# Kernel optimization log

Measured on AMD Instinct MI355X. Metric: run time of the kernel, lower is better.

## Reference

```python
import jax, jax.numpy as jnp
import numpy as np

BN_EPS = 1e-5


def setup_inputs() -> dict:
    key = jax.random.key(0)
    ks = jax.random.split(key, 12)
    N, E = 100000, 400000
    node_in, hidden, L = 32, 128, 4
    x = jax.random.normal(ks[0], (N, node_in), dtype=jnp.float32)
    edge_index = jax.random.randint(ks[1], (2, E), 0, N, dtype=jnp.int32)
    s = 1.0 / np.sqrt(node_in)
    emb_W = jax.random.uniform(ks[2], (node_in, hidden), minval=-s, maxval=s, dtype=jnp.float32)
    emb_b = jax.random.uniform(ks[3], (hidden,), minval=-s, maxval=s, dtype=jnp.float32)
    s1 = 1.0 / np.sqrt(hidden)
    s2 = 1.0 / np.sqrt(2 * hidden)
    W1 = jax.random.uniform(ks[4], (L, hidden, 2 * hidden), minval=-s1, maxval=s1, dtype=jnp.float32)
    b1 = jax.random.uniform(ks[5], (L, 2 * hidden), minval=-s1, maxval=s1, dtype=jnp.float32)
    W2 = jax.random.uniform(ks[6], (L, 2 * hidden, hidden), minval=-s2, maxval=s2, dtype=jnp.float32)
    b2 = jax.random.uniform(ks[7], (L, hidden), minval=-s2, maxval=s2, dtype=jnp.float32)
    gamma = jnp.ones((L, hidden), dtype=jnp.float32)
    beta = jnp.zeros((L, hidden), dtype=jnp.float32)
    return {"x": x, "edge_index": edge_index, "emb_W": emb_W, "emb_b": emb_b,
            "W1": W1, "b1": b1, "W2": W2, "b2": b2, "gamma": gamma, "beta": beta}


def reference(x, edge_index, emb_W, emb_b, W1, b1, W2, b2, gamma, beta):
    # Node embedding: [N, node_in] @ [node_in, H] -> [N, H]
    h = x @ emb_W + emb_b
    src, dst = edge_index[0], edge_index[1]
    N = h.shape[0]
    L = W1.shape[0]
    for l in range(L):
        # GINConv (eps=0): sum-aggregate neighbor features then add self
        agg = jax.ops.segment_sum(h[src], dst, num_segments=N)  # [N, H]
        z = h + agg
        # 2-layer MLP: H -> 2H -> H with ReLU
        z = jax.nn.relu(z @ W1[l] + b1[l]) @ W2[l] + b2[l]
        # BatchNorm1d over nodes (training-mode batch statistics)
        mean = jnp.mean(z, axis=0)
        var = jnp.var(z, axis=0)
        z = (z - mean) * jax.lax.rsqrt(var + BN_EPS) * gamma[l] + beta[l]
        # ReLU (dropout is identity in eval mode)
        h = jax.nn.relu(z)
    return h
```

## Files before the change

kernel.cpp:

```cpp
#include <hip/hip_runtime.h>

#define H 128
#define H2 256
#define NODE_IN 32
#define BN_EPS 1e-5f

typedef __bf16 bf16x8 __attribute__((ext_vector_type(8)));
typedef __bf16 bf16x4 __attribute__((ext_vector_type(4)));
typedef float f32x4 __attribute__((ext_vector_type(4)));

#define MFMA(a, b, c) __builtin_amdgcn_mfma_f32_16x16x32_bf16(a, b, c, 0, 0, 0)

__global__ __launch_bounds__(256) void convert_weights_kernel(
    const float* __restrict__ W1, const float* __restrict__ W2,
    const float* __restrict__ embW, char* __restrict__ Ws, int L)
{
    int idx = blockIdx.x * 256 + threadIdx.x;
    int per = H * H2;
    int total = L * per;
    if (idx < total) {
        int l = idx / per, r = idx % per;
        int k = r / H2, n = r % H2;
        int c = k >> 3, e = k & 7;
        size_t off = (size_t)l * 131072 + n * 256 + (((c ^ (n & 7)) << 4)) + e * 2;
        *(__bf16*)(Ws + off) = (__bf16)W1[idx];
    } else if (idx < 2 * total) {
        int j = idx - total;
        int l = j / per, r = j % per;
        int k = r / H, n = r % H;
        int c = k >> 3, e = k & 7;
        size_t off = (size_t)l * 131072 + 65536 + n * 512 + (((c ^ (n & 7)) << 4)) + e * 2;
        *(__bf16*)(Ws + off) = (__bf16)W2[j];
    } else if (idx < 2 * total + H * NODE_IN) {
        int j = idx - 2 * total;
        int k = j / H, c = j % H;
        size_t off = (size_t)L * 131072 + c * 64 + k * 2;
        *(__bf16*)(Ws + off) = (__bf16)embW[j];
    }
}

__global__ __launch_bounds__(512) void embed_kernel(
    const float* __restrict__ x, const char* __restrict__ Wse,
    const float* __restrict__ bias, __bf16* __restrict__ h, int N)
{
    int tid = threadIdx.x;
    int w = tid >> 6, lane = tid & 63;
    int l15 = lane & 15, kg = lane >> 4;

    bf16x8 aw[8];
#pragma unroll
    for (int nt = 0; nt < 8; ++nt)
        aw[nt] = *(const bf16x8*)(Wse + (nt * 16 + l15) * 64 + kg * 16);

    int r = (blockIdx.x * 8 + w) * 16 + l15;
    bool ok = (r < N);

    bf16x8 xb = {};
    if (ok) {
        float4 v0 = *(const float4*)&x[(size_t)r * NODE_IN + kg * 8];
        float4 v1 = *(const float4*)&x[(size_t)r * NODE_IN + kg * 8 + 4];
        xb[0] = (__bf16)v0.x; xb[1] = (__bf16)v0.y;
        xb[2] = (__bf16)v0.z; xb[3] = (__bf16)v0.w;
        xb[4] = (__bf16)v1.x; xb[5] = (__bf16)v1.y;
        xb[6] = (__bf16)v1.z; xb[7] = (__bf16)v1.w;
    }

    __bf16* hr = h + (size_t)r * H;
#pragma unroll
    for (int nt = 0; nt < 8; ++nt) {
        f32x4 acc = {0.f, 0.f, 0.f, 0.f};
        acc = MFMA(aw[nt], xb, acc);
        if (ok) {
            float4 bb = *(const float4*)&bias[nt * 16 + kg * 4];
            bf16x4 hv;
            hv[0] = (__bf16)(acc[0] + bb.x);
            hv[1] = (__bf16)(acc[1] + bb.y);
            hv[2] = (__bf16)(acc[2] + bb.z);
            hv[3] = (__bf16)(acc[3] + bb.w);
            *(bf16x4*)(hr + nt * 16 + kg * 4) = hv;
        }
    }
}

__global__ __launch_bounds__(256) void hist_kernel(
    const int* __restrict__ dst, int* __restrict__ deg, int E)
{
    int e = blockIdx.x * 256 + threadIdx.x;
    if (e < E) atomicAdd(&deg[dst[e]], 1);
}

__global__ __launch_bounds__(256) void scan_partial_kernel(
    const int* __restrict__ deg, int* __restrict__ bsum, int N)
{
    __shared__ int red[256];
    int b = blockIdx.x, t = threadIdx.x;
    int base = b * 2048 + t * 8;
    int s = 0;
#pragma unroll
    for (int i = 0; i < 8; ++i) { int idx = base + i; if (idx < N) s += deg[idx]; }
    red[t] = s;
    __syncthreads();
    for (int d = 128; d > 0; d >>= 1) {
        if (t < d) red[t] += red[t + d];
        __syncthreads();
    }
    if (t == 0) bsum[b] = red[0];
}

__global__ __launch_bounds__(256) void scan_bsum_kernel(
    int* __restrict__ bsum, int* __restrict__ total, int numB)
{
    __shared__ int ts[256];
    int t = threadIdx.x;
    int v = (t < numB) ? bsum[t] : 0;
    ts[t] = v;
    __syncthreads();
    for (int d = 1; d < 256; d <<= 1) {
        int u = (t >= d) ? ts[t - d] : 0;
        __syncthreads();
        ts[t] += u;
        __syncthreads();
    }
    if (t < numB) bsum[t] = ts[t] - v;
    if (t == 255) *total = ts[255];
}

__global__ __launch_bounds__(256) void scan_apply_kernel(
    const int* __restrict__ deg, const int* __restrict__ bsum,
    int* __restrict__ offp, int* __restrict__ cursor, int N)
{
    __shared__ int ts[256];
    int b = blockIdx.x, t = threadIdx.x;
    int base = b * 2048 + t * 8;
    int loc[8];
    int s = 0;
#pragma unroll
    for (int i = 0; i < 8; ++i) {
        int idx = base + i;
        loc[i] = (idx < N) ? deg[idx] : 0;
        s += loc[i];
    }
    ts[t] = s;
    __syncthreads();
    for (int d = 1; d < 256; d <<= 1) {
        int u = (t >= d) ? ts[t - d] : 0;
        __syncthreads();
        ts[t] += u;
        __syncthreads();
    }
    int run = bsum[b] + ts[t] - s;
#pragma unroll
    for (int i = 0; i < 8; ++i) {
        int idx = base + i;
        if (idx < N) { offp[idx] = run; cursor[idx] = run; }
        run += loc[i];
    }
}

__global__ __launch_bounds__(256) void fill_kernel(
    const int* __restrict__ src, const int* __restrict__ dst,
    int* __restrict__ cursor, int* __restrict__ srclist, int E)
{
    int e = blockIdx.x * 256 + threadIdx.x;
    if (e < E) {
        int pos = atomicAdd(&cursor[dst[e]], 1);
        srclist[pos] = src[e];
    }
}

__device__ __forceinline__ uint32_t pack_relu2(float x, float y) {
    __bf16 a = (__bf16)fmaxf(x, 0.f), b = (__bf16)fmaxf(y, 0.f);
    return (uint32_t)__builtin_bit_cast(uint16_t, a) |
           ((uint32_t)__builtin_bit_cast(uint16_t, b) << 16);
}

template <int BN>
__global__ __launch_bounds__(512, 4) void gin_layer_kernel(
    const __bf16* __restrict__ hin, __bf16* __restrict__ hout,
    const float* __restrict__ ss,
    const int* __restrict__ offp, const int* __restrict__ srclist,
    const char* __restrict__ Ws, const float* __restrict__ b1l,
    const float* __restrict__ b2l, float* __restrict__ spart, int N)
{
    __shared__ __align__(16) char zt[16384];
    __shared__ __align__(16) char hl[32768];
    __shared__ float sstat[256];

    int tid = threadIdx.x;
    int w = tid >> 6, lane = tid & 63;
    int l15 = lane & 15, kg = lane >> 4;
    const int xsw = (l15 & 7) << 4;
    int r0g = blockIdx.x * 64;

    if (tid < 256) sstat[tid] = 0.f;

    bf16x8 aW1[2][4];
#pragma unroll
    for (int nt = 0; nt < 2; ++nt)
#pragma unroll
        for (int kk = 0; kk < 4; ++kk)
            aW1[nt][kk] = *(const bf16x8*)(
                Ws + (w * 32 + nt * 16 + l15) * 256 + ((((kk * 4 + kg) << 4)) ^ xsw));
    float4 bb1[2];
#pragma unroll
    for (int nt = 0; nt < 2; ++nt)
        bb1[nt] = *(const float4*)&b1l[w * 32 + nt * 16 + kg * 4];

    {
        float sc[8], sh[8];
        if (BN) {
#pragma unroll
            for (int j = 0; j < 8; ++j) {
                sc[j] = ss[l15 * 8 + j];
                sh[j] = ss[H + l15 * 8 + j];
            }
        }
#pragma unroll
        for (int p = 0; p < 2; ++p) {
            int rl = w * 8 + p * 4 + kg;
            int r = r0g + rl;
            bf16x8 o = {};
            if (r < N) {
                float acc[8];
                bf16x8 sv = *(const bf16x8*)(hin + (size_t)r * H + l15 * 8);
#pragma unroll
                for (int j = 0; j < 8; ++j) {
                    float f = (float)sv[j];
                    acc[j] = BN ? fmaxf(f * sc[j] + sh[j], 0.f) : f;
                }
                int i0 = offp[r], i1 = offp[r + 1];
                int i = i0;
                for (; i + 3 < i1; i += 4) {
                    int s0 = srclist[i], s1 = srclist[i + 1];
                    int s2 = srclist[i + 2], s3 = srclist[i + 3];
                    bf16x8 u0 = *(const bf16x8*)(hin + (size_t)s0 * H + l15 * 8);
                    bf16x8 u1 = *(const bf16x8*)(hin + (size_t)s1 * H + l15 * 8);
                    bf16x8 u2 = *(const bf16x8*)(hin + (size_t)s2 * H + l15 * 8);
                    bf16x8 u3 = *(const bf16x8*)(hin + (size_t)s3 * H + l15 * 8);
#pragma unroll
                    for (int j = 0; j < 8; ++j) {
                        float f0 = (float)u0[j], f1 = (float)u1[j];
                        float f2 = (float)u2[j], f3 = (float)u3[j];
                        if (BN) {
                            f0 = fmaxf(f0 * sc[j] + sh[j], 0.f);
                            f1 = fmaxf(f1 * sc[j] + sh[j], 0.f);
                            f2 = fmaxf(f2 * sc[j] + sh[j], 0.f);
                            f3 = fmaxf(f3 * sc[j] + sh[j], 0.f);
                        }
                        acc[j] += (f0 + f1) + (f2 + f3);
                    }
                }
                for (; i < i1; ++i) {
                    int s0 = srclist[i];
                    bf16x8 u0 = *(const bf16x8*)(hin + (size_t)s0 * H + l15 * 8);
#pragma unroll
                    for (int j = 0; j < 8; ++j) {
                        float f0 = (float)u0[j];
                        if (BN) f0 = fmaxf(f0 * sc[j] + sh[j], 0.f);
                        acc[j] += f0;
                    }
                }
#pragma unroll
                for (int j = 0; j < 8; ++j) o[j] = (__bf16)acc[j];
            }
            int chunk = l15 ^ (rl & 7);
            *(bf16x8*)(zt + rl * 256 + chunk * 16) = o;
        }
    }
    __syncthreads();

#pragma unroll 1
    for (int i = 0; i < 4; ++i) {
        int rl = i * 16 + l15;
        bf16x8 zb[4];
#pragma unroll
        for (int kk = 0; kk < 4; ++kk)
            zb[kk] = *(const bf16x8*)(zt + rl * 256 + ((((kk * 4 + kg) << 4)) ^ xsw));
#pragma unroll
        for (int nt = 0; nt < 2; ++nt) {
            f32x4 a = {0.f, 0.f, 0.f, 0.f};
            a = MFMA(aW1[nt][0], zb[0], a);
            a = MFMA(aW1[nt][1], zb[1], a);
            a = MFMA(aW1[nt][2], zb[2], a);
            a = MFMA(aW1[nt][3], zb[3], a);
            uint32_t p0 = pack_relu2(a[0] + bb1[nt].x, a[1] + bb1[nt].y);
            uint32_t p1 = pack_relu2(a[2] + bb1[nt].z, a[3] + bb1[nt].w);
            int chunk = (w * 4 + nt * 2 + (kg >> 1)) ^ (l15 & 7);
            uint32_t* dstp = (uint32_t*)(hl + rl * 512 + chunk * 16 + (kg & 1) * 8);
            dstp[0] = p0;
            dstp[1] = p1;
        }
    }

    bf16x8 aW2[8];
#pragma unroll
    for (int kk = 0; kk < 8; ++kk)
        aW2[kk] = *(const bf16x8*)(
            Ws + 65536 + (w * 16 + l15) * 512 + ((((kk * 4 + kg) << 4)) ^ xsw));
    float4 bb2 = *(const float4*)&b2l[w * 16 + kg * 4];

    __syncthreads();

    float ps0 = 0.f, ps1 = 0.f, ps2 = 0.f, ps3 = 0.f;
    float pq0 = 0.f, pq1 = 0.f, pq2 = 0.f, pq3 = 0.f;
#pragma unroll 1
    for (int i = 0; i < 4; ++i) {
        int r = r0g + i * 16 + l15;
        bool ok = (r < N);
        int rl = i * 16 + l15;
        bf16x8 bd[8];
#pragma unroll
        for (int kk = 0; kk < 8; ++kk)
            bd[kk] = *(const bf16x8*)(hl + rl * 512 + ((((kk * 4 + kg) << 4)) ^ xsw));
        f32x4 c = {0.f, 0.f, 0.f, 0.f};
#pragma unroll
        for (int kk = 0; kk < 8; ++kk) c = MFMA(aW2[kk], bd[kk], c);
        if (ok) {
            float v0 = c[0] + bb2.x, v1 = c[1] + bb2.y;
            float v2 = c[2] + bb2.z, v3 = c[3] + bb2.w;
            bf16x4 ov;
            ov[0] = (__bf16)v0; ov[1] = (__bf16)v1;
            ov[2] = (__bf16)v2; ov[3] = (__bf16)v3;
            *(bf16x4*)(hout + (size_t)r * H + w * 16 + kg * 4) = ov;
            ps0 += v0; pq0 += v0 * v0;
            ps1 += v1; pq1 += v1 * v1;
            ps2 += v2; pq2 += v2 * v2;
            ps3 += v3; pq3 += v3 * v3;
        }
    }

    ps0 += __shfl_xor(ps0, 1, 64); ps0 += __shfl_xor(ps0, 2, 64);
    ps0 += __shfl_xor(ps0, 4, 64); ps0 += __shfl_xor(ps0, 8, 64);
    ps1 += __shfl_xor(ps1, 1, 64); ps1 += __shfl_xor(ps1, 2, 64);
    ps1 += __shfl_xor(ps1, 4, 64); ps1 += __shfl_xor(ps1, 8, 64);
    ps2 += __shfl_xor(ps2, 1, 64); ps2 += __shfl_xor(ps2, 2, 64);
    ps2 += __shfl_xor(ps2, 4, 64); ps2 += __shfl_xor(ps2, 8, 64);
    ps3 += __shfl_xor(ps3, 1, 64); ps3 += __shfl_xor(ps3, 2, 64);
    ps3 += __shfl_xor(ps3, 4, 64); ps3 += __shfl_xor(ps3, 8, 64);
    pq0 += __shfl_xor(pq0, 1, 64); pq0 += __shfl_xor(pq0, 2, 64);
    pq0 += __shfl_xor(pq0, 4, 64); pq0 += __shfl_xor(pq0, 8, 64);
    pq1 += __shfl_xor(pq1, 1, 64); pq1 += __shfl_xor(pq1, 2, 64);
    pq1 += __shfl_xor(pq1, 4, 64); pq1 += __shfl_xor(pq1, 8, 64);
    pq2 += __shfl_xor(pq2, 1, 64); pq2 += __shfl_xor(pq2, 2, 64);
    pq2 += __shfl_xor(pq2, 4, 64); pq2 += __shfl_xor(pq2, 8, 64);
    pq3 += __shfl_xor(pq3, 1, 64); pq3 += __shfl_xor(pq3, 2, 64);
    pq3 += __shfl_xor(pq3, 4, 64); pq3 += __shfl_xor(pq3, 8, 64);
    if (l15 == 0) {
        int cb = w * 16 + kg * 4;
        sstat[cb + 0] = ps0; sstat[cb + 1] = ps1;
        sstat[cb + 2] = ps2; sstat[cb + 3] = ps3;
        sstat[H + cb + 0] = pq0; sstat[H + cb + 1] = pq1;
        sstat[H + cb + 2] = pq2; sstat[H + cb + 3] = pq3;
    }
    __syncthreads();
    if (tid < 256) spart[(size_t)blockIdx.x * 256 + tid] = sstat[tid];
}

__global__ __launch_bounds__(256) void reduce_stats_kernel(
    const float* __restrict__ spart, float* __restrict__ stats, int R)
{
    int t = threadIdx.x;
    int b = blockIdx.x;
    int per = (R + gridDim.x - 1) / gridDim.x;
    int r0 = b * per, r1 = r0 + per;
    if (r1 > R) r1 = R;
    float s = 0.f;
    for (int r = r0; r < r1; ++r) s += spart[(size_t)r * 256 + t];
    atomicAdd(&stats[t], s);
}

__global__ void bn_finalize_kernel(const float* __restrict__ stats,
                                   const float* __restrict__ gamma,
                                   const float* __restrict__ beta,
                                   float* __restrict__ ss, int N)
{
    int j = threadIdx.x;
    float invN = 1.0f / (float)N;
    float mean = stats[j] * invN;
    float var = stats[H + j] * invN - mean * mean;
    float sc = gamma[j] * rsqrtf(var + BN_EPS);
    ss[j] = sc;
    ss[H + j] = beta[j] - mean * sc;
}

__global__ __launch_bounds__(256) void bn_apply_kernel(
    const __bf16* __restrict__ zpb, const float* __restrict__ ss,
    float* __restrict__ out, int N)
{
    size_t i = (size_t)blockIdx.x * 256 + threadIdx.x;
    size_t total = (size_t)N * (H / 8);
    if (i >= total) return;
    int c8 = (int)(i & (H / 8 - 1));
    bf16x8 v = *(const bf16x8*)(zpb + i * 8);
    float4 o0, o1;
    const float* scp = &ss[c8 * 8];
    const float* shp = &ss[H + c8 * 8];
    o0.x = fmaxf((float)v[0] * scp[0] + shp[0], 0.f);
    o0.y = fmaxf((float)v[1] * scp[1] + shp[1], 0.f);
    o0.z = fmaxf((float)v[2] * scp[2] + shp[2], 0.f);
    o0.w = fmaxf((float)v[3] * scp[3] + shp[3], 0.f);
    o1.x = fmaxf((float)v[4] * scp[4] + shp[4], 0.f);
    o1.y = fmaxf((float)v[5] * scp[5] + shp[5], 0.f);
    o1.z = fmaxf((float)v[6] * scp[6] + shp[6], 0.f);
    o1.w = fmaxf((float)v[7] * scp[7] + shp[7], 0.f);
    ((float4*)out)[i * 2] = o0;
    ((float4*)out)[i * 2 + 1] = o1;
}

static inline char* align_up(char* p, size_t a) {
    return (char*)(((uintptr_t)p + a - 1) & ~(uintptr_t)(a - 1));
}

extern "C" void kernel_launch(void* const* d_in, const int* in_sizes, int n_in,
                              void* d_out, int out_size, void* d_ws, size_t ws_size,
                              hipStream_t stream)
{
    const float* x    = (const float*)d_in[0];
    const int*   ei   = (const int*)d_in[1];
    const float* embW = (const float*)d_in[2];
    const float* embb = (const float*)d_in[3];
    const float* W1   = (const float*)d_in[4];
    const float* b1   = (const float*)d_in[5];
    const float* W2   = (const float*)d_in[6];
    const float* b2   = (const float*)d_in[7];
    const float* gamma= (const float*)d_in[8];
    const float* beta = (const float*)d_in[9];

    int N = in_sizes[0] / NODE_IN;
    int E = in_sizes[1] / 2;
    int L = in_sizes[4] / (H * H2);
    const int* src = ei;
    const int* dst = ei + E;

    int numB = (N + 2047) / 2048;
    int nblk = (N + 63) / 64;

    char* w = (char*)d_ws;
    __bf16* bufA = (__bf16*)w;   w += (size_t)N * H * sizeof(__bf16);
    w = align_up(w, 256);
    __bf16* bufB = (__bf16*)w;   w += (size_t)N * H * sizeof(__bf16);
    w = align_up(w, 256);
    float* spart = (float*)w;    w += (size_t)nblk * 256 * sizeof(float);
    float* statsAll = (float*)w; w += (size_t)L * 2 * H * sizeof(float);
    float* ss = (float*)w;       w += 2 * H * sizeof(float);
    int* deg = (int*)w;          w += (size_t)N * sizeof(int);
    int* offp = (int*)w;         w += (size_t)(N + 1) * sizeof(int);
    int* cursor = (int*)w;       w += (size_t)N * sizeof(int);
    int* bsum = (int*)w;         w += (size_t)numB * sizeof(int);
    int* srcl = (int*)w;         w += (size_t)E * sizeof(int);
    w = align_up(w, 256);
    char* Ws = w;                w += (size_t)L * 131072 + H * NODE_IN * 2;

    float* out = (float*)d_out;
    __bf16* buf[2] = {bufA, bufB};

    int wtotal = 2 * L * H * H2 + H * NODE_IN;
    convert_weights_kernel<<<(wtotal + 255) / 256, 256, 0, stream>>>(W1, W2, embW, Ws, L);
    embed_kernel<<<(N + 127) / 128, 512, 0, stream>>>(
        x, Ws + (size_t)L * 131072, embb, bufA, N);

    hipMemsetAsync(deg, 0, (size_t)N * sizeof(int), stream);
    hipMemsetAsync(statsAll, 0, (size_t)L * 2 * H * sizeof(float), stream);

    hist_kernel<<<(E + 255) / 256, 256, 0, stream>>>(dst, deg, E);
    scan_partial_kernel<<<numB, 256, 0, stream>>>(deg, bsum, N);
    scan_bsum_kernel<<<1, 256, 0, stream>>>(bsum, offp + N, numB);
    scan_apply_kernel<<<numB, 256, 0, stream>>>(deg, bsum, offp, cursor, N);
    fill_kernel<<<(E + 255) / 256, 256, 0, stream>>>(src, dst, cursor, srcl, E);

    int agrid = (int)(((size_t)N * (H / 8) + 255) / 256);

    for (int l = 0; l < L; ++l) {
        float* stats = statsAll + (size_t)l * 2 * H;
        const __bf16* hin = buf[l & 1];
        __bf16* hout = buf[(l + 1) & 1];
        if (l == 0)
            gin_layer_kernel<0><<<nblk, 512, 0, stream>>>(
                hin, hout, nullptr, offp, srcl,
                Ws + (size_t)l * 131072, b1 + (size_t)l * H2,
                b2 + (size_t)l * H, spart, N);
        else
            gin_layer_kernel<1><<<nblk, 512, 0, stream>>>(
                hin, hout, ss, offp, srcl,
                Ws + (size_t)l * 131072, b1 + (size_t)l * H2,
                b2 + (size_t)l * H, spart, N);
        reduce_stats_kernel<<<64, 256, 0, stream>>>(spart, stats, nblk);
        bn_finalize_kernel<<<1, H, 0, stream>>>(
            stats, gamma + (size_t)l * H, beta + (size_t)l * H, ss, N);
    }
    bn_apply_kernel<<<agrid, 256, 0, stream>>>(buf[L & 1], ss, out, N);
}
```

Baseline: 364.3 us.

## Unfuse BN+ReLU from gather into separate pass and halve rows per block

```diff
diff --git a/kernel.cpp b/kernel.cpp
--- a/kernel.cpp
+++ b/kernel.cpp
@@ -174,23 +174,21 @@
            ((uint32_t)__builtin_bit_cast(uint16_t, b) << 16);
 }
 
-template <int BN>
 __global__ __launch_bounds__(512, 4) void gin_layer_kernel(
-    const __bf16* __restrict__ hin, __bf16* __restrict__ hout,
-    const float* __restrict__ ss,
+    const __bf16* __restrict__ hin, __bf16* __restrict__ zpb,
     const int* __restrict__ offp, const int* __restrict__ srclist,
     const char* __restrict__ Ws, const float* __restrict__ b1l,
     const float* __restrict__ b2l, float* __restrict__ spart, int N)
 {
-    __shared__ __align__(16) char zt[16384];
-    __shared__ __align__(16) char hl[32768];
+    __shared__ __align__(16) char zt[8192];
+    __shared__ __align__(16) char hl[16384];
     __shared__ float sstat[256];
 
     int tid = threadIdx.x;
     int w = tid >> 6, lane = tid & 63;
     int l15 = lane & 15, kg = lane >> 4;
     const int xsw = (l15 & 7) << 4;
-    int r0g = blockIdx.x * 64;
+    int r0g = blockIdx.x * 32;
 
     if (tid < 256) sstat[tid] = 0.f;
 
@@ -207,70 +205,44 @@
         bb1[nt] = *(const float4*)&b1l[w * 32 + nt * 16 + kg * 4];
 
     {
-        float sc[8], sh[8];
-        if (BN) {
-#pragma unroll
-            for (int j = 0; j < 8; ++j) {
-                sc[j] = ss[l15 * 8 + j];
-                sh[j] = ss[H + l15 * 8 + j];
+        int rl = w * 4 + kg;
+        int r = r0g + rl;
+        bf16x8 o = {};
+        if (r < N) {
+            float acc[8];
+            bf16x8 sv = *(const bf16x8*)(hin + (size_t)r * H + l15 * 8);
+#pragma unroll
+            for (int j = 0; j < 8; ++j) acc[j] = (float)sv[j];
+            int i0 = offp[r], i1 = offp[r + 1];
+            int i = i0;
+            for (; i + 3 < i1; i += 4) {
+                int s0 = srclist[i], s1 = srclist[i + 1];
+                int s2 = srclist[i + 2], s3 = srclist[i + 3];
+                bf16x8 u0 = *(const bf16x8*)(hin + (size_t)s0 * H + l15 * 8);
+                bf16x8 u1 = *(const bf16x8*)(hin + (size_t)s1 * H + l15 * 8);
+                bf16x8 u2 = *(const bf16x8*)(hin + (size_t)s2 * H + l15 * 8);
+                bf16x8 u3 = *(const bf16x8*)(hin + (size_t)s3 * H + l15 * 8);
+#pragma unroll
+                for (int j = 0; j < 8; ++j)
+                    acc[j] += ((float)u0[j] + (float)u1[j]) +
+                              ((float)u2[j] + (float)u3[j]);
             }
+            for (; i < i1; ++i) {
+                int s0 = srclist[i];
+                bf16x8 u0 = *(const bf16x8*)(hin + (size_t)s0 * H + l15 * 8);
+#pragma unroll
+                for (int j = 0; j < 8; ++j) acc[j] += (float)u0[j];
+            }
+#pragma unroll
+            for (int j = 0; j < 8; ++j) o[j] = (__bf16)acc[j];
         }
-#pragma unroll
-        for (int p = 0; p < 2; ++p) {
-            int rl = w * 8 + p * 4 + kg;
-            int r = r0g + rl;
-            bf16x8 o = {};
-            if (r < N) {
-                float acc[8];
-                bf16x8 sv = *(const bf16x8*)(hin + (size_t)r * H + l15 * 8);
-#pragma unroll
-                for (int j = 0; j < 8; ++j) {
-                    float f = (float)sv[j];
-                    acc[j] = BN ? fmaxf(f * sc[j] + sh[j], 0.f) : f;
-                }
-                int i0 = offp[r], i1 = offp[r + 1];
-                int i = i0;
-                for (; i + 3 < i1; i += 4) {
-                    int s0 = srclist[i], s1 = srclist[i + 1];
-                    int s2 = srclist[i + 2], s3 = srclist[i + 3];
-                    bf16x8 u0 = *(const bf16x8*)(hin + (size_t)s0 * H + l15 * 8);
-                    bf16x8 u1 = *(const bf16x8*)(hin + (size_t)s1 * H + l15 * 8);
-                    bf16x8 u2 = *(const bf16x8*)(hin + (size_t)s2 * H + l15 * 8);
-                    bf16x8 u3 = *(const bf16x8*)(hin + (size_t)s3 * H + l15 * 8);
-#pragma unroll
-                    for (int j = 0; j < 8; ++j) {
-                        float f0 = (float)u0[j], f1 = (float)u1[j];
-                        float f2 = (float)u2[j], f3 = (float)u3[j];
-                        if (BN) {
-                            f0 = fmaxf(f0 * sc[j] + sh[j], 0.f);
-                            f1 = fmaxf(f1 * sc[j] + sh[j], 0.f);
-                            f2 = fmaxf(f2 * sc[j] + sh[j], 0.f);
-                            f3 = fmaxf(f3 * sc[j] + sh[j], 0.f);
-                        }
-                        acc[j] += (f0 + f1) + (f2 + f3);
-                    }
-                }
-                for (; i < i1; ++i) {
-                    int s0 = srclist[i];
-                    bf16x8 u0 = *(const bf16x8*)(hin + (size_t)s0 * H + l15 * 8);
-#pragma unroll
-                    for (int j = 0; j < 8; ++j) {
-                        float f0 = (float)u0[j];
-                        if (BN) f0 = fmaxf(f0 * sc[j] + sh[j], 0.f);
-                        acc[j] += f0;
-                    }
-                }
-#pragma unroll
-                for (int j = 0; j < 8; ++j) o[j] = (__bf16)acc[j];
-            }
-            int chunk = l15 ^ (rl & 7);
-            *(bf16x8*)(zt + rl * 256 + chunk * 16) = o;
-        }
+        int chunk = l15 ^ (rl & 7);
+        *(bf16x8*)(zt + rl * 256 + chunk * 16) = o;
     }
     __syncthreads();
 
 #pragma unroll 1
-    for (int i = 0; i < 4; ++i) {
+    for (int i = 0; i < 2; ++i) {
         int rl = i * 16 + l15;
         bf16x8 zb[4];
 #pragma unroll
@@ -304,7 +276,7 @@
     float ps0 = 0.f, ps1 = 0.f, ps2 = 0.f, ps3 = 0.f;
     float pq0 = 0.f, pq1 = 0.f, pq2 = 0.f, pq3 = 0.f;
 #pragma unroll 1
-    for (int i = 0; i < 4; ++i) {
+    for (int i = 0; i < 2; ++i) {
         int r = r0g + i * 16 + l15;
         bool ok = (r < N);
         int rl = i * 16 + l15;
@@ -321,7 +293,7 @@
             bf16x4 ov;
             ov[0] = (__bf16)v0; ov[1] = (__bf16)v1;
             ov[2] = (__bf16)v2; ov[3] = (__bf16)v3;
-            *(bf16x4*)(hout + (size_t)r * H + w * 16 + kg * 4) = ov;
+            *(bf16x4*)(zpb + (size_t)r * H + w * 16 + kg * 4) = ov;
             ps0 += v0; pq0 += v0 * v0;
             ps1 += v1; pq1 += v1 * v1;
             ps2 += v2; pq2 += v2 * v2;
@@ -383,6 +355,24 @@
     ss[H + j] = beta[j] - mean * sc;
 }
 
+__global__ __launch_bounds__(256) void bn_apply_bf16_kernel(
+    const __bf16* __restrict__ zpb, const float* __restrict__ ss,
+    __bf16* __restrict__ h, int N)
+{
+    size_t i = (size_t)blockIdx.x * 256 + threadIdx.x;
+    size_t total = (size_t)N * (H / 8);
+    if (i >= total) return;
+    int c8 = (int)(i & (H / 8 - 1));
+    bf16x8 v = *(const bf16x8*)(zpb + i * 8);
+    const float* scp = &ss[c8 * 8];
+    const float* shp = &ss[H + c8 * 8];
+    bf16x8 o;
+#pragma unroll
+    for (int j = 0; j < 8; ++j)
+        o[j] = (__bf16)fmaxf((float)v[j] * scp[j] + shp[j], 0.f);
+    *(bf16x8*)(h + i * 8) = o;
+}
+
 __global__ __launch_bounds__(256) void bn_apply_kernel(
     const __bf16* __restrict__ zpb, const float* __restrict__ ss,
     float* __restrict__ out, int N)
@@ -433,12 +423,12 @@
     const int* dst = ei + E;
 
     int numB = (N + 2047) / 2048;
-    int nblk = (N + 63) / 64;
+    int nblk = (N + 31) / 32;
 
     char* w = (char*)d_ws;
-    __bf16* bufA = (__bf16*)w;   w += (size_t)N * H * sizeof(__bf16);
+    __bf16* hbuf = (__bf16*)w;   w += (size_t)N * H * sizeof(__bf16);
     w = align_up(w, 256);
-    __bf16* bufB = (__bf16*)w;   w += (size_t)N * H * sizeof(__bf16);
+    __bf16* zpb = (__bf16*)w;    w += (size_t)N * H * sizeof(__bf16);
     w = align_up(w, 256);
     float* spart = (float*)w;    w += (size_t)nblk * 256 * sizeof(float);
     float* statsAll = (float*)w; w += (size_t)L * 2 * H * sizeof(float);
@@ -452,12 +442,11 @@
     char* Ws = w;                w += (size_t)L * 131072 + H * NODE_IN * 2;
 
     float* out = (float*)d_out;
-    __bf16* buf[2] = {bufA, bufB};
 
     int wtotal = 2 * L * H * H2 + H * NODE_IN;
     convert_weights_kernel<<<(wtotal + 255) / 256, 256, 0, stream>>>(W1, W2, embW, Ws, L);
     embed_kernel<<<(N + 127) / 128, 512, 0, stream>>>(
-        x, Ws + (size_t)L * 131072, embb, bufA, N);
+        x, Ws + (size_t)L * 131072, embb, hbuf, N);
 
     hipMemsetAsync(deg, 0, (size_t)N * sizeof(int), stream);
     hipMemsetAsync(statsAll, 0, (size_t)L * 2 * H * sizeof(float), stream);
@@ -472,21 +461,16 @@
 
     for (int l = 0; l < L; ++l) {
         float* stats = statsAll + (size_t)l * 2 * H;
-        const __bf16* hin = buf[l & 1];
-        __bf16* hout = buf[(l + 1) & 1];
-        if (l == 0)
-            gin_layer_kernel<0><<<nblk, 512, 0, stream>>>(
-                hin, hout, nullptr, offp, srcl,
-                Ws + (size_t)l * 131072, b1 + (size_t)l * H2,
-                b2 + (size_t)l * H, spart, N);
-        else
-            gin_layer_kernel<1><<<nblk, 512, 0, stream>>>(
-                hin, hout, ss, offp, srcl,
-                Ws + (size_t)l * 131072, b1 + (size_t)l * H2,
-                b2 + (size_t)l * H, spart, N);
+        gin_layer_kernel<<<nblk, 512, 0, stream>>>(
+            hbuf, zpb, offp, srcl,
+            Ws + (size_t)l * 131072, b1 + (size_t)l * H2,
+            b2 + (size_t)l * H, spart, N);
         reduce_stats_kernel<<<64, 256, 0, stream>>>(spart, stats, nblk);
         bn_finalize_kernel<<<1, H, 0, stream>>>(
             stats, gamma + (size_t)l * H, beta + (size_t)l * H, ss, N);
-    }
-    bn_apply_kernel<<<agrid, 256, 0, stream>>>(buf[L & 1], ss, out, N);
-}
+        if (l < L - 1)
+            bn_apply_bf16_kernel<<<agrid, 256, 0, stream>>>(zpb, ss, hbuf, N);
+        else
+            bn_apply_kernel<<<agrid, 256, 0, stream>>>(zpb, ss, out, N);
+    }
+}
```

Measured after the change: 435.5 us. 19.5% more time.

## Fold BN finalize into consumer kernels and prefetch both rows' offsets

Applied to the files above, without the earlier changes.

```diff
diff --git a/kernel.cpp b/kernel.cpp
--- a/kernel.cpp
+++ b/kernel.cpp
@@ -177,14 +177,14 @@
 template <int BN>
 __global__ __launch_bounds__(512, 4) void gin_layer_kernel(
     const __bf16* __restrict__ hin, __bf16* __restrict__ hout,
-    const float* __restrict__ ss,
+    const float* __restrict__ stats, const float* __restrict__ gammaP,
+    const float* __restrict__ betaP, float invN,
     const int* __restrict__ offp, const int* __restrict__ srclist,
     const char* __restrict__ Ws, const float* __restrict__ b1l,
     const float* __restrict__ b2l, float* __restrict__ spart, int N)
 {
     __shared__ __align__(16) char zt[16384];
     __shared__ __align__(16) char hl[32768];
-    __shared__ float sstat[256];
 
     int tid = threadIdx.x;
     int w = tid >> 6, lane = tid & 63;
@@ -192,8 +192,6 @@
     const int xsw = (l15 & 7) << 4;
     int r0g = blockIdx.x * 64;
 
-    if (tid < 256) sstat[tid] = 0.f;
-
     bf16x8 aW1[2][4];
 #pragma unroll
     for (int nt = 0; nt < 2; ++nt)
@@ -206,31 +204,45 @@
     for (int nt = 0; nt < 2; ++nt)
         bb1[nt] = *(const float4*)&b1l[w * 32 + nt * 16 + kg * 4];
 
+    float sc[8], sh[8];
+    if (BN) {
+#pragma unroll
+        for (int j = 0; j < 8; ++j) {
+            int c = l15 * 8 + j;
+            float mean = stats[c] * invN;
+            float var = stats[H + c] * invN - mean * mean;
+            float s = gammaP[c] * rsqrtf(var + BN_EPS);
+            sc[j] = s;
+            sh[j] = betaP[c] - mean * s;
+        }
+    }
+
     {
-        float sc[8], sh[8];
-        if (BN) {
-#pragma unroll
-            for (int j = 0; j < 8; ++j) {
-                sc[j] = ss[l15 * 8 + j];
-                sh[j] = ss[H + l15 * 8 + j];
-            }
-        }
-#pragma unroll
-        for (int p = 0; p < 2; ++p) {
-            int rl = w * 8 + p * 4 + kg;
-            int r = r0g + rl;
+        int rlA = w * 8 + kg, rlB = rlA + 4;
+        int rA = r0g + rlA, rB = r0g + rlB;
+        bool okA = (rA < N), okB = (rB < N);
+        int iA0 = 0, iA1 = 0, iB0 = 0, iB1 = 0;
+        bf16x8 svA = {}, svB = {};
+        if (okA) {
+            iA0 = offp[rA]; iA1 = offp[rA + 1];
+            svA = *(const bf16x8*)(hin + (size_t)rA * H + l15 * 8);
+        }
+        if (okB) {
+            iB0 = offp[rB]; iB1 = offp[rB + 1];
+            svB = *(const bf16x8*)(hin + (size_t)rB * H + l15 * 8);
+        }
+
+        {
             bf16x8 o = {};
-            if (r < N) {
+            if (okA) {
                 float acc[8];
-                bf16x8 sv = *(const bf16x8*)(hin + (size_t)r * H + l15 * 8);
 #pragma unroll
                 for (int j = 0; j < 8; ++j) {
-                    float f = (float)sv[j];
+                    float f = (float)svA[j];
                     acc[j] = BN ? fmaxf(f * sc[j] + sh[j], 0.f) : f;
                 }
-                int i0 = offp[r], i1 = offp[r + 1];
-                int i = i0;
-                for (; i + 3 < i1; i += 4) {
+                int i = iA0;
+                for (; i + 3 < iA1; i += 4) {
                     int s0 = srclist[i], s1 = srclist[i + 1];
                     int s2 = srclist[i + 2], s3 = srclist[i + 3];
                     bf16x8 u0 = *(const bf16x8*)(hin + (size_t)s0 * H + l15 * 8);
@@ -250,7 +262,7 @@
                         acc[j] += (f0 + f1) + (f2 + f3);
                     }
                 }
-                for (; i < i1; ++i) {
+                for (; i < iA1; ++i) {
                     int s0 = srclist[i];
                     bf16x8 u0 = *(const bf16x8*)(hin + (size_t)s0 * H + l15 * 8);
 #pragma unroll
@@ -263,8 +275,55 @@
 #pragma unroll
                 for (int j = 0; j < 8; ++j) o[j] = (__bf16)acc[j];
             }
-            int chunk = l15 ^ (rl & 7);
-            *(bf16x8*)(zt + rl * 256 + chunk * 16) = o;
+            int chunk = l15 ^ (rlA & 7);
+            *(bf16x8*)(zt + rlA * 256 + chunk * 16) = o;
+        }
+
+        {
+            bf16x8 o = {};
+            if (okB) {
+                float acc[8];
+#pragma unroll
+                for (int j = 0; j < 8; ++j) {
+                    float f = (float)svB[j];
+                    acc[j] = BN ? fmaxf(f * sc[j] + sh[j], 0.f) : f;
+                }
+                int i = iB0;
+                for (; i + 3 < iB1; i += 4) {
+                    int s0 = srclist[i], s1 = srclist[i + 1];
+                    int s2 = srclist[i + 2], s3 = srclist[i + 3];
+                    bf16x8 u0 = *(const bf16x8*)(hin + (size_t)s0 * H + l15 * 8);
+                    bf16x8 u1 = *(const bf16x8*)(hin + (size_t)s1 * H + l15 * 8);
+                    bf16x8 u2 = *(const bf16x8*)(hin + (size_t)s2 * H + l15 * 8);
+                    bf16x8 u3 = *(const bf16x8*)(hin + (size_t)s3 * H + l15 * 8);
+#pragma unroll
+                    for (int j = 0; j < 8; ++j) {
+                        float f0 = (float)u0[j], f1 = (float)u1[j];
+                        float f2 = (float)u2[j], f3 = (float)u3[j];
+                        if (BN) {
+                            f0 = fmaxf(f0 * sc[j] + sh[j], 0.f);
+                            f1 = fmaxf(f1 * sc[j] + sh[j], 0.f);
+                            f2 = fmaxf(f2 * sc[j] + sh[j], 0.f);
+                            f3 = fmaxf(f3 * sc[j] + sh[j], 0.f);
+                        }
+                        acc[j] += (f0 + f1) + (f2 + f3);
+                    }
+                }
+                for (; i < iB1; ++i) {
+                    int s0 = srclist[i];
+                    bf16x8 u0 = *(const bf16x8*)(hin + (size_t)s0 * H + l15 * 8);
+#pragma unroll
+                    for (int j = 0; j < 8; ++j) {
+                        float f0 = (float)u0[j];
+                        if (BN) f0 = fmaxf(f0 * sc[j] + sh[j], 0.f);
+                        acc[j] += f0;
+                    }
+                }
+#pragma unroll
+                for (int j = 0; j < 8; ++j) o[j] = (__bf16)acc[j];
+            }
+            int chunk = l15 ^ (rlB & 7);
+            *(bf16x8*)(zt + rlB * 256 + chunk * 16) = o;
         }
     }
     __syncthreads();
@@ -346,14 +405,11 @@
     pq3 += __shfl_xor(pq3, 1, 64); pq3 += __shfl_xor(pq3, 2, 64);
     pq3 += __shfl_xor(pq3, 4, 64); pq3 += __shfl_xor(pq3, 8, 64);
     if (l15 == 0) {
+        size_t row = (size_t)blockIdx.x * 256;
         int cb = w * 16 + kg * 4;
-        sstat[cb + 0] = ps0; sstat[cb + 1] = ps1;
-        sstat[cb + 2] = ps2; sstat[cb + 3] = ps3;
-        sstat[H + cb + 0] = pq0; sstat[H + cb + 1] = pq1;
-        sstat[H + cb + 2] = pq2; sstat[H + cb + 3] = pq3;
-    }
-    __syncthreads();
-    if (tid < 256) spart[(size_t)blockIdx.x * 256 + tid] = sstat[tid];
+        *(float4*)&spart[row + cb] = make_float4(ps0, ps1, ps2, ps3);
+        *(float4*)&spart[row + H + cb] = make_float4(pq0, pq1, pq2, pq3);
+    }
 }
 
 __global__ __launch_bounds__(256) void reduce_stats_kernel(
@@ -369,23 +425,10 @@
     atomicAdd(&stats[t], s);
 }
 
-__global__ void bn_finalize_kernel(const float* __restrict__ stats,
-                                   const float* __restrict__ gamma,
-                                   const float* __restrict__ beta,
-                                   float* __restrict__ ss, int N)
-{
-    int j = threadIdx.x;
-    float invN = 1.0f / (float)N;
-    float mean = stats[j] * invN;
-    float var = stats[H + j] * invN - mean * mean;
-    float sc = gamma[j] * rsqrtf(var + BN_EPS);
-    ss[j] = sc;
-    ss[H + j] = beta[j] - mean * sc;
-}
-
 __global__ __launch_bounds__(256) void bn_apply_kernel(
-    const __bf16* __restrict__ zpb, const float* __restrict__ ss,
-    float* __restrict__ out, int N)
+    const __bf16* __restrict__ zpb, const float* __restrict__ stats,
+    const float* __restrict__ gammaP, const float* __restrict__ betaP,
+    float invN, float* __restrict__ out, int N)
 {
     size_t i = (size_t)blockIdx.x * 256 + threadIdx.x;
     size_t total = (size_t)N * (H / 8);
@@ -393,16 +436,18 @@
     int c8 = (int)(i & (H / 8 - 1));
     bf16x8 v = *(const bf16x8*)(zpb + i * 8);
     float4 o0, o1;
-    const float* scp = &ss[c8 * 8];
-    const float* shp = &ss[H + c8 * 8];
-    o0.x = fmaxf((float)v[0] * scp[0] + shp[0], 0.f);
-    o0.y = fmaxf((float)v[1] * scp[1] + shp[1], 0.f);
-    o0.z = fmaxf((float)v[2] * scp[2] + shp[2], 0.f);
-    o0.w = fmaxf((float)v[3] * scp[3] + shp[3], 0.f);
-    o1.x = fmaxf((float)v[4] * scp[4] + shp[4], 0.f);
-    o1.y = fmaxf((float)v[5] * scp[5] + shp[5], 0.f);
-    o1.z = fmaxf((float)v[6] * scp[6] + shp[6], 0.f);
-    o1.w = fmaxf((float)v[7] * scp[7] + shp[7], 0.f);
+    float o[8];
+#pragma unroll
+    for (int j = 0; j < 8; ++j) {
+        int c = c8 * 8 + j;
+        float mean = stats[c] * invN;
+        float var = stats[H + c] * invN - mean * mean;
+        float s = gammaP[c] * rsqrtf(var + BN_EPS);
+        float sh = betaP[c] - mean * s;
+        o[j] = fmaxf((float)v[j] * s + sh, 0.f);
+    }
+    o0.x = o[0]; o0.y = o[1]; o0.z = o[2]; o0.w = o[3];
+    o1.x = o[4]; o1.y = o[5]; o1.z = o[6]; o1.w = o[7];
     ((float4*)out)[i * 2] = o0;
     ((float4*)out)[i * 2 + 1] = o1;
 }
@@ -431,6 +476,7 @@
     int L = in_sizes[4] / (H * H2);
     const int* src = ei;
     const int* dst = ei + E;
+    float invN = 1.0f / (float)N;
 
     int numB = (N + 2047) / 2048;
     int nblk = (N + 63) / 64;
@@ -442,7 +488,6 @@
     w = align_up(w, 256);
     float* spart = (float*)w;    w += (size_t)nblk * 256 * sizeof(float);
     float* statsAll = (float*)w; w += (size_t)L * 2 * H * sizeof(float);
-    float* ss = (float*)w;       w += 2 * H * sizeof(float);
     int* deg = (int*)w;          w += (size_t)N * sizeof(int);
     int* offp = (int*)w;         w += (size_t)(N + 1) * sizeof(int);
     int* cursor = (int*)w;       w += (size_t)N * sizeof(int);
@@ -476,17 +521,19 @@
         __bf16* hout = buf[(l + 1) & 1];
         if (l == 0)
             gin_layer_kernel<0><<<nblk, 512, 0, stream>>>(
-                hin, hout, nullptr, offp, srcl,
+                hin, hout, nullptr, nullptr, nullptr, 0.f, offp, srcl,
                 Ws + (size_t)l * 131072, b1 + (size_t)l * H2,
                 b2 + (size_t)l * H, spart, N);
         else
             gin_layer_kernel<1><<<nblk, 512, 0, stream>>>(
-                hin, hout, ss, offp, srcl,
+                hin, hout, statsAll + (size_t)(l - 1) * 2 * H,
+                gamma + (size_t)(l - 1) * H, beta + (size_t)(l - 1) * H, invN,
+                offp, srcl,
                 Ws + (size_t)l * 131072, b1 + (size_t)l * H2,
                 b2 + (size_t)l * H, spart, N);
         reduce_stats_kernel<<<64, 256, 0, stream>>>(spart, stats, nblk);
-        bn_finalize_kernel<<<1, H, 0, stream>>>(
-            stats, gamma + (size_t)l * H, beta + (size_t)l * H, ss, N);
-    }
-    bn_apply_kernel<<<agrid, 256, 0, stream>>>(buf[L & 1], ss, out, N);
-}
+    }
+    bn_apply_kernel<<<agrid, 256, 0, stream>>>(
+        buf[L & 1], statsAll + (size_t)(L - 1) * 2 * H,
+        gamma + (size_t)(L - 1) * H, beta + (size_t)(L - 1) * H, invN, out, N);
+}
```

Result: no change. 364.5 us (+0.0%).
